# Performance work log

Measured on AMD Instinct MI355X. Metric: run time of the kernel, lower is better.

## Reference

```python
import jax, jax.numpy as jnp
import numpy as np

HIDDEN = 4544
NUM_HEADS = 71
HEAD_DIM = 64
ROPE_BASE = 10000.0


def _rope_cos_sin(seq_len, dim, dtype):
    inv_freq = 1.0 / (ROPE_BASE ** (jnp.arange(0, dim, 2, dtype=jnp.float32) / dim))
    t = jnp.arange(seq_len, dtype=jnp.float32)
    freqs = jnp.einsum('i,j->ij', t, inv_freq)            # [S, dim/2]
    emb = jnp.concatenate([freqs, freqs], axis=-1)        # [S, dim]
    return jnp.cos(emb).astype(dtype), jnp.sin(emb).astype(dtype)


def _rotate_half(x):
    half = x.shape[-1] // 2
    return jnp.concatenate([-x[..., half:], x[..., :half]], axis=-1)


def _apply_rope(x, cos, sin):
    # x: [..., S, hd]; cos/sin: [S, hd]
    return x * cos + _rotate_half(x) * sin


def setup_inputs() -> dict:
    key = jax.random.key(0)
    k1, k2, k3 = jax.random.split(key, 3)
    B, S = 1, 1024
    hidden_states = jax.random.normal(k1, (B, 1, S, HIDDEN), dtype=jnp.float32) * 0.02
    # additive causal mask (prefill)
    neg = jnp.triu(jnp.full((S, S), -1e9, dtype=jnp.float32), k=1)
    attention_mask = jnp.broadcast_to(neg[None, None], (B, 1, S, S))
    # fused QKV weight (already transposed for right-matmul): [H, (nh+2)*hd]
    qkv_w = jax.random.normal(k2, (HIDDEN, (NUM_HEADS + 2) * HEAD_DIM), dtype=jnp.float32) * 0.02
    dense_w = jax.random.normal(k3, (HIDDEN, HIDDEN), dtype=jnp.float32) * 0.02
    return {"hidden_states": hidden_states, "attention_mask": attention_mask,
            "qkv_w": qkv_w, "dense_w": dense_w}


def reference(hidden_states, attention_mask, qkv_w, dense_w):
    B, _, S, H = hidden_states.shape
    nh, hd = NUM_HEADS, HEAD_DIM
    x = hidden_states[:, 0]                               # [B, S, H]
    fused = jnp.einsum('bsh,hf->bsf', x, qkv_w)           # [B, S, (nh+2)*hd]
    fused = fused.reshape(B, S, nh + 2, hd)
    q = jnp.transpose(fused[:, :, :nh, :], (0, 2, 1, 3))  # [B, nh, S, hd]
    k = fused[:, :, nh, :]                                # [B, S, hd]  (single KV head, MQA)
    v = fused[:, :, nh + 1, :]                            # [B, S, hd]
    cos, sin = _rope_cos_sin(S, hd, q.dtype)
    q = _apply_rope(q, cos, sin)
    k = _apply_rope(k, cos, sin)
    scale = 1.0 / np.sqrt(hd).astype(np.float32)
    scores = jnp.einsum('bhsd,btd->bhst', q, k) * scale   # [B, nh, S, S]
    scores = scores + attention_mask                      # broadcast over heads
    probs = jax.nn.softmax(scores, axis=-1)
    ctx = jnp.einsum('bhst,btd->bhsd', probs, v)          # [B, nh, S, hd]
    ctx = jnp.transpose(ctx, (0, 2, 1, 3)).reshape(B, S, nh * hd)
    out = jnp.einsum('bsh,hg->bsg', ctx, dense_w)         # [B, S, H]
    return out[:, None]                                   # [B, 1, S, H]
```

## Files before the change

### kernel.cpp

```cpp
#include <hip/hip_runtime.h>

#define S_LEN 1024
#define HID   4544
#define NH    71
#define NQKV  4672

typedef __attribute__((ext_vector_type(4)))  float f32x4;
typedef __attribute__((ext_vector_type(16))) float f32x16;
typedef __attribute__((ext_vector_type(4))) unsigned short u16x4;
typedef __attribute__((ext_vector_type(8))) unsigned short u16x8;
typedef __attribute__((ext_vector_type(8))) __bf16 bf16x8;

__device__ __forceinline__ bf16x8 as_bf(u16x8 v) { return __builtin_bit_cast(bf16x8, v); }

__device__ __forceinline__ unsigned short f2bf(float f) {
    unsigned u = __builtin_bit_cast(unsigned, f);
    return (unsigned short)((u + 0x7FFFu + ((u >> 16) & 1u)) >> 16);
}
__device__ __forceinline__ float bf2f(unsigned short u) {
    return __builtin_bit_cast(float, (unsigned)u << 16);
}
__device__ __forceinline__ unsigned pk2(float a, float b) {
    return (unsigned)f2bf(a) | ((unsigned)f2bf(b) << 16);
}
__device__ __forceinline__ void gload16(const void* g, void* l) {
    __builtin_amdgcn_global_load_lds((const __attribute__((address_space(1))) unsigned int*)g,
                                     (__attribute__((address_space(3))) unsigned int*)l,
                                     16, 0, 0);
}

__global__ __launch_bounds__(256) void cvt_x_kernel(const float4* __restrict__ x,
                                                    ushort4* __restrict__ y) {
    int i = blockIdx.x * 256 + threadIdx.x;
    float4 v = x[i];
    ushort4 r;
    r.x = f2bf(v.x); r.y = f2bf(v.y); r.z = f2bf(v.z); r.w = f2bf(v.w);
    y[i] = r;
}

__global__ __launch_bounds__(256) void cvt_wT_kernel(const float* __restrict__ w,
                                                     unsigned short* __restrict__ wt,
                                                     int K, int N) {
    __shared__ float t[64][65];
    int n0 = blockIdx.x * 64, k0 = blockIdx.y * 64;
    int tx = threadIdx.x & 15, ty = threadIdx.x >> 4;
#pragma unroll
    for (int r = 0; r < 64; r += 16) {
        int k = k0 + ty + r;
        float4 v = *(const float4*)&w[(size_t)k * N + n0 + tx * 4];
        t[ty + r][tx * 4 + 0] = v.x;
        t[ty + r][tx * 4 + 1] = v.y;
        t[ty + r][tx * 4 + 2] = v.z;
        t[ty + r][tx * 4 + 3] = v.w;
    }
    __syncthreads();
    int nr = threadIdx.x >> 2;
    int kq = (threadIdx.x & 3) * 16;
    unsigned short tmp[16];
#pragma unroll
    for (int z = 0; z < 16; z++) tmp[z] = f2bf(t[kq + z][nr]);
    u16x8* dst = (u16x8*)&wt[(size_t)(n0 + nr) * K + k0 + kq];
    dst[0] = *(const u16x8*)&tmp[0];
    dst[1] = *(const u16x8*)&tmp[8];
}

__global__ void rope_table_kernel(float* __restrict__ cs, float* __restrict__ sn) {
    int s = blockIdx.x, i = threadIdx.x;
    float inv = powf(10000.0f, -(2.0f * (float)i) / 64.0f);
    float f = (float)s * inv;
    cs[s * 32 + i] = cosf(f);
    sn[s * 32 + i] = sinf(f);
}

template<int EPI>
__global__ __launch_bounds__(128, 2) void gemm_bt_kernel(
        const unsigned short* __restrict__ A, const unsigned short* __restrict__ BT,
        void* __restrict__ Cout, const float* __restrict__ cs_t,
        const float* __restrict__ sn_t, unsigned short* __restrict__ k_out,
        unsigned short* __restrict__ v_out, int K, int ldc) {
    __shared__ unsigned short As[2][128 * 64];
    __shared__ unsigned short Bs[2][64 * 64];
    int p = blockIdx.x;
    int per = gridDim.x >> 3;
    int l = (p & 7) * per + (p >> 3);
    int m0 = (l & 7) * 128, ni_b = l >> 3, n0 = ni_b * 64;
    int t = threadIdx.x;
    int wv = t >> 6, lane = t & 63;
    int lrow = lane & 31;
    int lk   = lane >> 5;
    int mw = wv * 64;

    f32x16 acc[2][2];
#pragma unroll
    for (int mi = 0; mi < 2; mi++)
#pragma unroll
        for (int ni = 0; ni < 2; ni++) acc[mi][ni] = (f32x16)0.0f;

    const char* Ab = (const char*)A;
    const char* Bb = (const char*)BT;
    size_t rs = (size_t)K * 2;

    auto stage = [&](int step, int buf) {
        size_t kb = (size_t)step * 128;
#pragma unroll
        for (int i = 0; i < 8; i++) {
            int chunk = i * 128 + t;
            int row = chunk >> 3, c16 = chunk & 7;
            int csrc = c16 ^ (row & 7);
            gload16(Ab + (size_t)(m0 + row) * rs + kb + csrc * 16,
                    (char*)As[buf] + chunk * 16);
        }
#pragma unroll
        for (int i = 0; i < 4; i++) {
            int chunk = i * 128 + t;
            int row = chunk >> 3, c16 = chunk & 7;
            int csrc = c16 ^ (row & 7);
            gload16(Bb + (size_t)(n0 + row) * rs + kb + csrc * 16,
                    (char*)Bs[buf] + chunk * 16);
        }
    };

    int nsteps = K >> 6;
    stage(0, 0);
    if (nsteps > 1) stage(1, 1);
    for (int s = 0; s < nsteps; ++s) {
        int cur = s & 1;
        if (s + 1 < nsteps) { asm volatile("s_waitcnt vmcnt(12)" ::: "memory"); }
        else                { asm volatile("s_waitcnt vmcnt(0)" ::: "memory"); }
        __builtin_amdgcn_s_barrier();
        bf16x8 af[2][4], bfr[2][4];
#pragma unroll
        for (int mi = 0; mi < 2; mi++) {
            int row = mw + mi * 32 + lrow;
#pragma unroll
            for (int kk = 0; kk < 4; kk++)
                af[mi][kk] = as_bf(*(const u16x8*)&As[cur][row * 64 + (((kk * 2 + lk) ^ (row & 7)) << 3)]);
        }
#pragma unroll
        for (int ni = 0; ni < 2; ni++) {
            int row = ni * 32 + lrow;
#pragma unroll
            for (int kk = 0; kk < 4; kk++)
                bfr[ni][kk] = as_bf(*(const u16x8*)&Bs[cur][row * 64 + (((kk * 2 + lk) ^ (row & 7)) << 3)]);
        }
        asm volatile("s_waitcnt lgkmcnt(0)" ::: "memory");
        __builtin_amdgcn_s_barrier();
        if (s + 2 < nsteps) stage(s + 2, cur);
#pragma unroll
        for (int kk = 0; kk < 4; kk++)
#pragma unroll
            for (int mi = 0; mi < 2; mi++)
#pragma unroll
                for (int ni = 0; ni < 2; ni++)
                    acc[mi][ni] = __builtin_amdgcn_mfma_f32_32x32x16_bf16(
                        af[mi][kk], bfr[ni][kk], acc[mi][ni], 0, 0, 0);
    }

    if (EPI == 0) {
        float* C = (float*)Cout;
#pragma unroll
        for (int mi = 0; mi < 2; mi++)
#pragma unroll
            for (int ni = 0; ni < 2; ni++) {
                int col = n0 + ni * 32 + lrow;
#pragma unroll
                for (int r = 0; r < 16; r++) {
                    int row = m0 + mw + mi * 32 + (r & 3) + 8 * (r >> 2) + 4 * lk;
                    C[(size_t)row * ldc + col] = acc[mi][ni][r];
                }
            }
    } else {
        int hh = ni_b;
        if (hh == 72) {
#pragma unroll
            for (int mi = 0; mi < 2; mi++)
#pragma unroll
                for (int ni = 0; ni < 2; ni++) {
                    int d = ni * 32 + lrow;
#pragma unroll
                    for (int g = 0; g < 4; g++) {
                        int s0 = m0 + mw + mi * 32 + 8 * g + 4 * lk;
                        u16x4 pk;
#pragma unroll
                        for (int i = 0; i < 4; i++) pk[i] = f2bf(acc[mi][ni][g * 4 + i]);
                        *(u16x4*)&v_out[(size_t)d * S_LEN + s0] = pk;
                    }
                }
        } else {
            unsigned short* qb = (unsigned short*)Cout;
            float qscale = (hh < 71) ? 0.125f : 1.0f;
#pragma unroll
            for (int mi = 0; mi < 2; mi++)
#pragma unroll
                for (int r = 0; r < 16; r++) {
                    int s = m0 + mw + mi * 32 + (r & 3) + 8 * (r >> 2) + 4 * lk;
                    float c = cs_t[s * 32 + lrow];
                    float g = sn_t[s * 32 + lrow];
                    float x0 = acc[mi][0][r];
                    float x1 = acc[mi][1][r];
                    float r0 = (x0 * c - x1 * g) * qscale;
                    float r1 = (x1 * c + x0 * g) * qscale;
                    if (hh < 71) {
                        qb[(size_t)s * HID + hh * 64 + lrow]      = f2bf(r0);
                        qb[(size_t)s * HID + hh * 64 + 32 + lrow] = f2bf(r1);
                    } else {
                        k_out[(size_t)s * 64 + lrow]      = f2bf(r0);
                        k_out[(size_t)s * 64 + 32 + lrow] = f2bf(r1);
                    }
                }
        }
    }
}

__global__ __launch_bounds__(256, 3) void attn_kernel(
        const unsigned short* __restrict__ qb, const unsigned short* __restrict__ kr,
        const unsigned short* __restrict__ vt, unsigned short* __restrict__ ctx,
        unsigned short* __restrict__ Opart, float2* __restrict__ MLpart) {
    __shared__ unsigned short Ks[2][64 * 64];
    __shared__ unsigned short Vs[2][64 * 64];
    __shared__ unsigned short Pl[4][16 * 72];
    int h = blockIdx.y;
    int u = blockIdx.x;
    int c, j0;
    if (u < 16)      { c = 0; j0 = u * 4; }
    else if (u < 28) { c = 1; j0 = 16 + (u - 16) * 4; }
    else if (u < 36) { c = 2; j0 = 32 + (u - 28) * 4; }
    else             { c = 3; j0 = 48 + (u - 36) * 4; }
    int t = threadIdx.x, wv = t >> 6, lane = t & 63, lr = lane & 15, lg = lane >> 4;
    int j = j0 + wv;
    int qs = j * 16 + lr;
    int k_lo = c * 256;
    int kend_w   = min((j + 1) * 16, k_lo + 256);
    int kend_max = min((j0 + 4) * 16, k_lo + 256);
    int nt = (kend_max - k_lo) >> 6;
    int nch = (j >> 4) + 1;
    int srow = t >> 3, sc16 = t & 7, sw = lr & 7;

    auto stage = [&](int ti, int buf) {
        size_t kbase = (size_t)(k_lo + ti * 64);
#pragma unroll
        for (int i = 0; i < 2; i++) {
            int row = i * 32 + srow;
            int csrc = sc16 ^ (row & 7);
            gload16((const char*)kr + (kbase + row) * 128 + csrc * 16,
                    (char*)Ks[buf] + (i * 256 + t) * 16);
        }
#pragma unroll
        for (int i = 0; i < 2; i++) {
            int row = i * 32 + srow;
            int csrc = sc16 ^ (row & 7);
            gload16((const char*)vt + (size_t)row * 2048 + kbase * 2 + csrc * 16,
                    (char*)Vs[buf] + (i * 256 + t) * 16);
        }
    };

    bf16x8 qf[2];
#pragma unroll
    for (int dc = 0; dc < 2; dc++)
        qf[dc] = as_bf(*(const u16x8*)&qb[(size_t)qs * HID + h * 64 + dc * 32 + 8 * lg]);

    float m_i = -1e30f, l_i = 0.0f;
    f32x4 o[4];
#pragma unroll
    for (int d4 = 0; d4 < 4; d4++) o[d4] = (f32x4)0.0f;

    stage(0, 0);
    if (nt > 1) stage(1, 1);

    for (int ti = 0; ti < nt; ti++) {
        int cur = ti & 1;
        if (ti + 1 < nt) { asm volatile("s_waitcnt vmcnt(4)" ::: "memory"); }
        else             { asm volatile("s_waitcnt vmcnt(0)" ::: "memory"); }
        __builtin_amdgcn_s_barrier();
        int k0 = k_lo + ti * 64;
        if (k0 < kend_w) {
            f32x4 st[4];
#pragma unroll
            for (int nc = 0; nc < 4; nc++) st[nc] = (f32x4)0.0f;
#pragma unroll
            for (int nc = 0; nc < 4; nc++) {
                int krow = nc * 16 + lr;
#pragma unroll
                for (int dc = 0; dc < 2; dc++) {
                    bf16x8 kf = as_bf(*(const u16x8*)&Ks[cur][krow * 64 + (((dc * 4 + lg) ^ sw) << 3)]);
                    st[nc] = __builtin_amdgcn_mfma_f32_16x16x32_bf16(kf, qf[dc], st[nc], 0, 0, 0);
                }
            }
            bool needmask = (k0 + 64 > j * 16);
            float mx = -1e30f;
            if (needmask) {
#pragma unroll
                for (int nc = 0; nc < 4; nc++)
#pragma unroll
                    for (int i = 0; i < 4; i++) {
                        int ks = k0 + nc * 16 + 4 * lg + i;
                        float v = (ks <= qs) ? st[nc][i] : -1e30f;
                        st[nc][i] = v;
                        mx = fmaxf(mx, v);
                    }
            } else {
#pragma unroll
                for (int nc = 0; nc < 4; nc++)
#pragma unroll
                    for (int i = 0; i < 4; i++) mx = fmaxf(mx, st[nc][i]);
            }
            mx = fmaxf(mx, __shfl_xor(mx, 16));
            mx = fmaxf(mx, __shfl_xor(mx, 32));
            if (!__all(mx <= m_i + 8.0f)) {
                float mn = fmaxf(m_i, mx);
                float so = __expf(m_i - mn);
                l_i *= so;
#pragma unroll
                for (int d4 = 0; d4 < 4; d4++)
#pragma unroll
                    for (int i = 0; i < 4; i++) o[d4][i] *= so;
                m_i = mn;
            }
            float ps = 0.0f;
#pragma unroll
            for (int nc = 0; nc < 4; nc++)
#pragma unroll
                for (int i = 0; i < 4; i++) {
                    float v = st[nc][i];
                    float e = (!needmask || v > -1e29f) ? __expf(v - m_i) : 0.0f;
                    st[nc][i] = e;
                    ps += e;
                }
            ps += __shfl_xor(ps, 16);
            ps += __shfl_xor(ps, 32);
            l_i += ps;
#pragma unroll
            for (int nc = 0; nc < 4; nc++) {
                *(unsigned*)&Pl[wv][lr * 72 + nc * 16 + 4 * lg]     = pk2(st[nc][0], st[nc][1]);
                *(unsigned*)&Pl[wv][lr * 72 + nc * 16 + 4 * lg + 2] = pk2(st[nc][2], st[nc][3]);
            }
            bf16x8 pb[2];
#pragma unroll
            for (int kk = 0; kk < 2; kk++)
                pb[kk] = as_bf(*(const u16x8*)&Pl[wv][lr * 72 + kk * 32 + 8 * lg]);
#pragma unroll
            for (int d4 = 0; d4 < 4; d4++) {
                int vrow = d4 * 16 + lr;
#pragma unroll
                for (int kk = 0; kk < 2; kk++) {
                    bf16x8 vf = as_bf(*(const u16x8*)&Vs[cur][vrow * 64 + (((kk * 4 + lg) ^ sw) << 3)]);
                    o[d4] = __builtin_amdgcn_mfma_f32_16x16x32_bf16(vf, pb[kk], o[d4], 0, 0, 0);
                }
            }
        }
        __builtin_amdgcn_s_barrier();
        if (ti + 2 < nt) stage(ti + 2, cur);
    }

    if (nch == 1) {
        float linv = 1.0f / l_i;
#pragma unroll
        for (int d4 = 0; d4 < 4; d4++) {
            u16x4 pk;
#pragma unroll
            for (int i = 0; i < 4; i++) pk[i] = f2bf(o[d4][i] * linv);
            *(u16x4*)&ctx[(size_t)qs * HID + h * 64 + d4 * 16 + 4 * lg] = pk;
        }
    } else {
        int pi = (h * 48 + (j - 16)) * 4 + c;
#pragma unroll
        for (int d4 = 0; d4 < 4; d4++) {
            u16x4 pk;
#pragma unroll
            for (int i = 0; i < 4; i++) pk[i] = f2bf(o[d4][i]);
            *(u16x4*)&Opart[(size_t)pi * 1024 + lr * 64 + d4 * 16 + 4 * lg] = pk;
        }
        if (lg == 0) MLpart[pi * 16 + lr] = make_float2(m_i, l_i);
    }
}

__global__ __launch_bounds__(256) void merge_kernel(
        const unsigned short* __restrict__ Opart, const float2* __restrict__ MLpart,
        unsigned short* __restrict__ ctx) {
    int mu = blockIdx.x * 4 + (threadIdx.x >> 6);
    int lane = threadIdx.x & 63;
    int h = mu / 48, jj = mu % 48, j = 16 + jj;
    int nch = (j >> 4) + 1;
    int base = (h * 48 + jj) * 4;
    for (int q = 0; q < 16; q++) {
        float m[4], l[4], w[4];
        float M = -1e30f;
        for (int c = 0; c < nch; c++) {
            float2 ml = MLpart[(base + c) * 16 + q];
            m[c] = ml.x; l[c] = ml.y;
            M = fmaxf(M, m[c]);
        }
        float L = 0.0f;
        for (int c = 0; c < nch; c++) { w[c] = __expf(m[c] - M); L += l[c] * w[c]; }
        float acc = 0.0f;
        for (int c = 0; c < nch; c++)
            acc += w[c] * bf2f(Opart[(size_t)(base + c) * 1024 + q * 64 + lane]);
        ctx[(size_t)(j * 16 + q) * HID + h * 64 + lane] = f2bf(acc / L);
    }
}

extern "C" void kernel_launch(void* const* d_in, const int* in_sizes, int n_in,
                              void* d_out, int out_size, void* d_ws, size_t ws_size,
                              hipStream_t stream) {
    const float* hs      = (const float*)d_in[0];
    const float* qkv_w   = (const float*)d_in[2];
    const float* dense_w = (const float*)d_in[3];
    float* out = (float*)d_out;

    char* ws = (char*)d_ws;
    size_t off = 0;
    auto alloc = [&](size_t bytes) -> void* {
        void* p = ws + off;
        off += (bytes + 255) & ~(size_t)255;
        return p;
    };
    unsigned short* x_bf   = (unsigned short*)alloc((size_t)S_LEN * HID * 2);
    unsigned short* wqkvT  = (unsigned short*)alloc((size_t)NQKV * HID * 2);
    unsigned short* q_bf   = (unsigned short*)alloc((size_t)S_LEN * HID * 2);
    unsigned short* k_rope = (unsigned short*)alloc((size_t)S_LEN * 64 * 2);
    unsigned short* v_t    = (unsigned short*)alloc((size_t)64 * S_LEN * 2);
    unsigned short* ctx    = (unsigned short*)alloc((size_t)S_LEN * HID * 2);
    unsigned short* wdT    = (unsigned short*)alloc((size_t)HID * HID * 2);
    float*          cs_t   = (float*)alloc((size_t)S_LEN * 32 * 4);
    float*          sn_t   = (float*)alloc((size_t)S_LEN * 32 * 4);
    (void)ws_size;
    unsigned short* Opart  = wqkvT;
    float2*         MLpart = (float2*)((char*)wqkvT + (size_t)71 * 48 * 4 * 1024 * 2);

    cvt_x_kernel<<<dim3(S_LEN * HID / 1024), dim3(256), 0, stream>>>(
        (const float4*)hs, (ushort4*)x_bf);
    cvt_wT_kernel<<<dim3(NQKV / 64, HID / 64), dim3(256), 0, stream>>>(
        qkv_w, wqkvT, HID, NQKV);
    cvt_wT_kernel<<<dim3(HID / 64, HID / 64), dim3(256), 0, stream>>>(
        dense_w, wdT, HID, HID);
    rope_table_kernel<<<dim3(S_LEN), dim3(32), 0, stream>>>(cs_t, sn_t);

    gemm_bt_kernel<1><<<dim3(NQKV / 64 * 8), dim3(128), 0, stream>>>(
        x_bf, wqkvT, q_bf, cs_t, sn_t, k_rope, v_t, HID, HID);

    attn_kernel<<<dim3(40, NH), dim3(256), 0, stream>>>(
        q_bf, k_rope, v_t, ctx, Opart, MLpart);

    merge_kernel<<<dim3(NH * 48 / 4), dim3(256), 0, stream>>>(Opart, MLpart, ctx);

    gemm_bt_kernel<0><<<dim3(HID / 64 * 8), dim3(128), 0, stream>>>(
        ctx, wdT, out, nullptr, nullptr, nullptr, nullptr, HID, HID);
}
```

Before: 296.4 us.

## Retile GEMMs to 128x128 blocks with four waves and padded weight transposes

Changes the bf16 GEMM from 128x64 tiles with two waves and K-step 64 to 128x128 tiles with four waves in a 2x2 layout and K-step 32. Weight transposes are padded to multiples of 128 columns with zero fill, and stores are masked against the true width. The aim is higher arithmetic intensity per block and fewer blocks re-reading A. In exchange each block runs more pipeline iterations with smaller per-step loads, grid size drops, and the padded columns do wasted compute.

```diff
diff --git a/kernel.cpp b/kernel.cpp
--- a/kernel.cpp
+++ b/kernel.cpp
@@ -4,6 +4,8 @@
 #define HID   4544
 #define NH    71
 #define NQKV  4672
+#define NQKV_PAD 4736
+#define ND_PAD   4608
 
 typedef __attribute__((ext_vector_type(4)))  float f32x4;
 typedef __attribute__((ext_vector_type(16))) float f32x16;
@@ -47,7 +49,9 @@
 #pragma unroll
     for (int r = 0; r < 64; r += 16) {
         int k = k0 + ty + r;
-        float4 v = *(const float4*)&w[(size_t)k * N + n0 + tx * 4];
+        int n = n0 + tx * 4;
+        float4 v = make_float4(0.f, 0.f, 0.f, 0.f);
+        if (n < N) v = *(const float4*)&w[(size_t)k * N + n];
         t[ty + r][tx * 4 + 0] = v.x;
         t[ty + r][tx * 4 + 1] = v.y;
         t[ty + r][tx * 4 + 2] = v.z;
@@ -73,22 +77,23 @@
 }
 
 template<int EPI>
-__global__ __launch_bounds__(128, 2) void gemm_bt_kernel(
+__global__ __launch_bounds__(256, 4) void gemm_bt_kernel(
         const unsigned short* __restrict__ A, const unsigned short* __restrict__ BT,
         void* __restrict__ Cout, const float* __restrict__ cs_t,
         const float* __restrict__ sn_t, unsigned short* __restrict__ k_out,
-        unsigned short* __restrict__ v_out, int K, int ldc) {
-    __shared__ unsigned short As[2][128 * 64];
-    __shared__ unsigned short Bs[2][64 * 64];
+        unsigned short* __restrict__ v_out, int K, int ldc, int n_store) {
+    __shared__ unsigned short As[2][128 * 32];
+    __shared__ unsigned short Bs[2][128 * 32];
     int p = blockIdx.x;
     int per = gridDim.x >> 3;
     int l = (p & 7) * per + (p >> 3);
-    int m0 = (l & 7) * 128, ni_b = l >> 3, n0 = ni_b * 64;
+    int m0 = (l & 7) * 128;
+    int nb = l >> 3;
+    int n0 = nb * 128;
     int t = threadIdx.x;
     int wv = t >> 6, lane = t & 63;
-    int lrow = lane & 31;
-    int lk   = lane >> 5;
-    int mw = wv * 64;
+    int wm = wv >> 1, wn = wv & 1;
+    int lrow = lane & 31, lk = lane >> 5;
 
     f32x16 acc[2][2];
 #pragma unroll
@@ -101,53 +106,53 @@
     size_t rs = (size_t)K * 2;
 
     auto stage = [&](int step, int buf) {
-        size_t kb = (size_t)step * 128;
-#pragma unroll
-        for (int i = 0; i < 8; i++) {
-            int chunk = i * 128 + t;
-            int row = chunk >> 3, c16 = chunk & 7;
-            int csrc = c16 ^ (row & 7);
+        size_t kb = (size_t)step * 64;
+#pragma unroll
+        for (int i = 0; i < 2; i++) {
+            int chunk = i * 256 + t;
+            int row = chunk >> 2, c4 = chunk & 3;
+            int csrc = c4 ^ (row & 3);
             gload16(Ab + (size_t)(m0 + row) * rs + kb + csrc * 16,
                     (char*)As[buf] + chunk * 16);
         }
 #pragma unroll
-        for (int i = 0; i < 4; i++) {
-            int chunk = i * 128 + t;
-            int row = chunk >> 3, c16 = chunk & 7;
-            int csrc = c16 ^ (row & 7);
+        for (int i = 0; i < 2; i++) {
+            int chunk = i * 256 + t;
+            int row = chunk >> 2, c4 = chunk & 3;
+            int csrc = c4 ^ (row & 3);
             gload16(Bb + (size_t)(n0 + row) * rs + kb + csrc * 16,
                     (char*)Bs[buf] + chunk * 16);
         }
     };
 
-    int nsteps = K >> 6;
+    int nsteps = K >> 5;
     stage(0, 0);
     if (nsteps > 1) stage(1, 1);
     for (int s = 0; s < nsteps; ++s) {
         int cur = s & 1;
-        if (s + 1 < nsteps) { asm volatile("s_waitcnt vmcnt(12)" ::: "memory"); }
+        if (s + 1 < nsteps) { asm volatile("s_waitcnt vmcnt(4)" ::: "memory"); }
         else                { asm volatile("s_waitcnt vmcnt(0)" ::: "memory"); }
         __builtin_amdgcn_s_barrier();
-        bf16x8 af[2][4], bfr[2][4];
+        bf16x8 af[2][2], bfr[2][2];
 #pragma unroll
         for (int mi = 0; mi < 2; mi++) {
-            int row = mw + mi * 32 + lrow;
-#pragma unroll
-            for (int kk = 0; kk < 4; kk++)
-                af[mi][kk] = as_bf(*(const u16x8*)&As[cur][row * 64 + (((kk * 2 + lk) ^ (row & 7)) << 3)]);
+            int row = wm * 64 + mi * 32 + lrow;
+#pragma unroll
+            for (int kk = 0; kk < 2; kk++)
+                af[mi][kk] = as_bf(*(const u16x8*)&As[cur][row * 32 + (((kk * 2 + lk) ^ (row & 3)) << 3)]);
         }
 #pragma unroll
         for (int ni = 0; ni < 2; ni++) {
-            int row = ni * 32 + lrow;
-#pragma unroll
-            for (int kk = 0; kk < 4; kk++)
-                bfr[ni][kk] = as_bf(*(const u16x8*)&Bs[cur][row * 64 + (((kk * 2 + lk) ^ (row & 7)) << 3)]);
+            int row = wn * 64 + ni * 32 + lrow;
+#pragma unroll
+            for (int kk = 0; kk < 2; kk++)
+                bfr[ni][kk] = as_bf(*(const u16x8*)&Bs[cur][row * 32 + (((kk * 2 + lk) ^ (row & 3)) << 3)]);
         }
         asm volatile("s_waitcnt lgkmcnt(0)" ::: "memory");
         __builtin_amdgcn_s_barrier();
         if (s + 2 < nsteps) stage(s + 2, cur);
 #pragma unroll
-        for (int kk = 0; kk < 4; kk++)
+        for (int kk = 0; kk < 2; kk++)
 #pragma unroll
             for (int mi = 0; mi < 2; mi++)
 #pragma unroll
@@ -162,15 +167,17 @@
         for (int mi = 0; mi < 2; mi++)
 #pragma unroll
             for (int ni = 0; ni < 2; ni++) {
-                int col = n0 + ni * 32 + lrow;
-#pragma unroll
-                for (int r = 0; r < 16; r++) {
-                    int row = m0 + mw + mi * 32 + (r & 3) + 8 * (r >> 2) + 4 * lk;
-                    C[(size_t)row * ldc + col] = acc[mi][ni][r];
+                int col = n0 + wn * 64 + ni * 32 + lrow;
+                if (col < n_store) {
+#pragma unroll
+                    for (int r = 0; r < 16; r++) {
+                        int row = m0 + wm * 64 + mi * 32 + (r & 3) + 8 * (r >> 2) + 4 * lk;
+                        C[(size_t)row * ldc + col] = acc[mi][ni][r];
+                    }
                 }
             }
     } else {
-        int hh = ni_b;
+        int hh = nb * 2 + wn;
         if (hh == 72) {
 #pragma unroll
             for (int mi = 0; mi < 2; mi++)
@@ -179,21 +186,21 @@
                     int d = ni * 32 + lrow;
 #pragma unroll
                     for (int g = 0; g < 4; g++) {
-                        int s0 = m0 + mw + mi * 32 + 8 * g + 4 * lk;
+                        int s0 = m0 + wm * 64 + mi * 32 + 8 * g + 4 * lk;
                         u16x4 pk;
 #pragma unroll
                         for (int i = 0; i < 4; i++) pk[i] = f2bf(acc[mi][ni][g * 4 + i]);
                         *(u16x4*)&v_out[(size_t)d * S_LEN + s0] = pk;
                     }
                 }
-        } else {
+        } else if (hh < 72) {
             unsigned short* qb = (unsigned short*)Cout;
             float qscale = (hh < 71) ? 0.125f : 1.0f;
 #pragma unroll
             for (int mi = 0; mi < 2; mi++)
 #pragma unroll
                 for (int r = 0; r < 16; r++) {
-                    int s = m0 + mw + mi * 32 + (r & 3) + 8 * (r >> 2) + 4 * lk;
+                    int s = m0 + wm * 64 + mi * 32 + (r & 3) + 8 * (r >> 2) + 4 * lk;
                     float c = cs_t[s * 32 + lrow];
                     float g = sn_t[s * 32 + lrow];
                     float x0 = acc[mi][0][r];
@@ -415,12 +422,12 @@
         return p;
     };
     unsigned short* x_bf   = (unsigned short*)alloc((size_t)S_LEN * HID * 2);
-    unsigned short* wqkvT  = (unsigned short*)alloc((size_t)NQKV * HID * 2);
+    unsigned short* wqkvT  = (unsigned short*)alloc((size_t)NQKV_PAD * HID * 2);
     unsigned short* q_bf   = (unsigned short*)alloc((size_t)S_LEN * HID * 2);
     unsigned short* k_rope = (unsigned short*)alloc((size_t)S_LEN * 64 * 2);
     unsigned short* v_t    = (unsigned short*)alloc((size_t)64 * S_LEN * 2);
     unsigned short* ctx    = (unsigned short*)alloc((size_t)S_LEN * HID * 2);
-    unsigned short* wdT    = (unsigned short*)alloc((size_t)HID * HID * 2);
+    unsigned short* wdT    = (unsigned short*)alloc((size_t)ND_PAD * HID * 2);
     float*          cs_t   = (float*)alloc((size_t)S_LEN * 32 * 4);
     float*          sn_t   = (float*)alloc((size_t)S_LEN * 32 * 4);
     (void)ws_size;
@@ -429,20 +436,20 @@
 
     cvt_x_kernel<<<dim3(S_LEN * HID / 1024), dim3(256), 0, stream>>>(
         (const float4*)hs, (ushort4*)x_bf);
-    cvt_wT_kernel<<<dim3(NQKV / 64, HID / 64), dim3(256), 0, stream>>>(
+    cvt_wT_kernel<<<dim3(NQKV_PAD / 64, HID / 64), dim3(256), 0, stream>>>(
         qkv_w, wqkvT, HID, NQKV);
-    cvt_wT_kernel<<<dim3(HID / 64, HID / 64), dim3(256), 0, stream>>>(
+    cvt_wT_kernel<<<dim3(ND_PAD / 64, HID / 64), dim3(256), 0, stream>>>(
         dense_w, wdT, HID, HID);
     rope_table_kernel<<<dim3(S_LEN), dim3(32), 0, stream>>>(cs_t, sn_t);
 
-    gemm_bt_kernel<1><<<dim3(NQKV / 64 * 8), dim3(128), 0, stream>>>(
-        x_bf, wqkvT, q_bf, cs_t, sn_t, k_rope, v_t, HID, HID);
+    gemm_bt_kernel<1><<<dim3(NQKV_PAD / 128 * 8), dim3(256), 0, stream>>>(
+        x_bf, wqkvT, q_bf, cs_t, sn_t, k_rope, v_t, HID, HID, NQKV);
 
     attn_kernel<<<dim3(40, NH), dim3(256), 0, stream>>>(
         q_bf, k_rope, v_t, ctx, Opart, MLpart);
 
     merge_kernel<<<dim3(NH * 48 / 4), dim3(256), 0, stream>>>(Opart, MLpart, ctx);
 
-    gemm_bt_kernel<0><<<dim3(HID / 64 * 8), dim3(128), 0, stream>>>(
-        ctx, wdT, out, nullptr, nullptr, nullptr, nullptr, HID, HID);
-}
+    gemm_bt_kernel<0><<<dim3(ND_PAD / 128 * 8), dim3(256), 0, stream>>>(
+        ctx, wdT, out, nullptr, nullptr, nullptr, nullptr, HID, HID, HID);
+}
```

Result: slower. 329.2 us (+11.1%).
